# Performance work log

Hardware: AMD Instinct MI355X
Metric: run time of the kernel (lower is better)

## Reference

```python
import jax, jax.numpy as jnp
import numpy as np

RANK = 64          # rank
ENT_COMPS = 5      # ent_comps (1 time + 4 space components per rank slot)
REL_COMPS = 4      # rel_comps (quaternion / boost velocity)
N_ENT = 80000
N_REL = 500
B = 2000
INIT_SIZE = 0.001
SCALE = 1.0 / np.sqrt(RANK)
EPS = 1e-9


def _quat_mul(q, p):
    # Hamilton product of quaternions q, p: [..., 4] each, layout (w, x, y, z)
    qw, qx, qy, qz = q[..., 0], q[..., 1], q[..., 2], q[..., 3]
    pw, px, py, pz = p[..., 0], p[..., 1], p[..., 2], p[..., 3]
    return jnp.stack([
        qw * pw - qx * px - qy * py - qz * pz,
        qw * px + qx * pw + qy * pz - qz * py,
        qw * py - qx * pz + qy * pw + qz * px,
        qw * pz + qx * py - qy * px + qz * pw,
    ], axis=-1)


def lorentz_rotate(x, r):
    # x: [B, R, 5] Lorentz vectors (t, s4); r: [B, R, 4] rotation quaternion.
    # Spatial 4D isoclinic rotation via unit-quaternion left multiplication; time fixed.
    q = r * jax.lax.rsqrt(jnp.sum(r * r, axis=-1, keepdims=True) + EPS)
    t, s = x[..., :1], x[..., 1:]
    return jnp.concatenate([t, _quat_mul(q, s)], axis=-1)


def lorentz_boost(x, v):
    # x: [B, R, 5]; v: [B, R, 4] boost velocity (|v| < 1).
    t, s = x[..., :1], x[..., 1:]
    vn2 = jnp.clip(jnp.sum(v * v, axis=-1, keepdims=True), 0.0, 0.999)  # [B,R,1]
    gamma = jax.lax.rsqrt(1.0 - vn2)
    vs = jnp.sum(v * s, axis=-1, keepdims=True)
    t2 = gamma * (t + vs)
    s2 = s + (gamma * t + (gamma - 1.0) * vs / (vn2 + EPS)) * v
    return jnp.concatenate([t2, s2], axis=-1)


def setup_inputs() -> dict:
    key = jax.random.key(0)
    k = jax.random.split(key, 6)
    queries = jax.random.randint(k[0], (B, 3), 0, N_REL, dtype=jnp.int32)
    stru_entities = jax.random.normal(k[1], (N_ENT, 2 * RANK, ENT_COMPS), jnp.float32) * INIT_SIZE
    stru_rel_rotate = jax.random.normal(k[2], (N_REL, RANK, REL_COMPS), jnp.float32) * INIT_SIZE
    stru_rel_boosts = jax.random.normal(k[3], (N_REL, RANK, REL_COMPS), jnp.float32) * INIT_SIZE
    stru_atten = jax.random.normal(k[4], (N_REL, 1, ENT_COMPS * RANK), jnp.float32) * INIT_SIZE
    stru_rel_aux = jax.random.normal(k[5], (N_REL, 2, ENT_COMPS * RANK), jnp.float32) * INIT_SIZE
    return {
        "queries": queries,
        "stru_entities": stru_entities,
        "stru_rel_rotate": stru_rel_rotate,
        "stru_rel_boosts": stru_rel_boosts,
        "stru_atten": stru_atten,
        "stru_rel_aux": stru_rel_aux,
    }


def reference(queries, stru_entities, stru_rel_rotate, stru_rel_boosts, stru_atten, stru_rel_aux):
    b = queries.shape[0]
    D = ENT_COMPS * RANK  # 320
    h, r, t = queries[:, 0], queries[:, 1], queries[:, 2]

    slhs = stru_entities[h]                       # [B, 2R, 5]
    srhs = stru_entities[t]                       # [B, 2R, 5]
    lhs_re = slhs[:, :RANK]                       # [B, R, 5]
    lhs_im = slhs[:, RANK:].reshape(b, D)         # [B, D]
    rhs_re = srhs[:, :RANK].reshape(b, D)
    rhs_im = srhs[:, RANK:].reshape(b, D)

    rrot = stru_rel_rotate[r]                     # [B, R, 4]
    rboost = stru_rel_boosts[r]                   # [B, R, 4]
    atten = stru_atten[r]                         # [B, 1, D]
    aux = stru_rel_aux[r]                         # [B, 2, D]
    aux0, aux1 = aux[:, 0], aux[:, 1]

    to_re = stru_entities[:, :RANK].reshape(N_ENT, D)
    to_im = stru_entities[:, RANK:].reshape(N_ENT, D)

    rot = lorentz_rotate(lhs_re, rrot).reshape(b, D, 1)
    boo = lorentz_boost(lhs_re, rboost).reshape(b, D, 1)
    cands = jnp.concatenate([rot, boo], axis=-1)              # [B, D, 2]
    weights = jax.nn.softmax(jnp.matmul(atten * SCALE, cands), axis=-1)  # [B, 1, 2]
    lhs = jnp.sum(cands * weights, axis=-1)                   # [B, D]

    scores = (lhs * aux0 - lhs_im * aux1) @ to_re.T \
           + (lhs * aux1 + lhs_im * aux0) @ to_im.T           # [B, N_ENT]

    reg0 = jnp.sqrt(lhs_re.reshape(b, D) ** 2 + lhs_im ** 2)
    reg1 = jnp.sqrt(aux0 ** 2 + aux1 ** 2)
    reg2 = jnp.sqrt(rhs_re ** 2 + rhs_im ** 2) * (1.0 / 3.0)
    reg3 = jnp.sqrt(jnp.sum(rrot ** 2, axis=-1))
    reg4 = jnp.sqrt(jnp.sum(rboost ** 2, axis=-1))
    return scores, reg0, reg1, reg2, reg3, reg4
```

## Files before the change

kernel.cpp:

```cpp
#include <hip/hip_runtime.h>
#include <math.h>

#define RANK 64
#define D_DIM 320
#define K_DIM 640
#define N_ENT 80000
#define B_Q 2000
#define M_PAD 2048
#define NBLK_N 313
#define NT 10
#define SCALE_F 0.125f
#define EPS_F 1e-9f

#define OFF_SCORES 0ull
#define OFF_REG0 160000000ull
#define OFF_REG1 160640000ull
#define OFF_REG2 161280000ull
#define OFF_REG3 161920000ull
#define OFF_REG4 162048000ull

typedef __attribute__((ext_vector_type(8))) short short8v;
typedef __attribute__((ext_vector_type(4))) float floatx4;

typedef __attribute__((address_space(1))) const unsigned int gu32;
typedef __attribute__((address_space(3))) unsigned int lu32;

#define VMCNT4() asm volatile("s_waitcnt vmcnt(4)" ::: "memory")
#define VMCNT0() asm volatile("s_waitcnt vmcnt(0)" ::: "memory")
#define LGKM0()  asm volatile("s_waitcnt lgkmcnt(0)" ::: "memory")

static __device__ __forceinline__ unsigned short f2bf(float f) {
    union { float f; unsigned int u; } a; a.f = f;
    unsigned int u = a.u;
    u += 0x7FFFu + ((u >> 16) & 1u);
    return (unsigned short)(u >> 16);
}

static __device__ __forceinline__ void prep_row(
    int b, int lane,
    const int* __restrict__ q,
    const float* __restrict__ ent,
    const float* __restrict__ rrot_t,
    const float* __restrict__ rboost_t,
    const float* __restrict__ atten_t,
    const float* __restrict__ aux_t,
    unsigned short* __restrict__ X,
    float* __restrict__ out)
{
    unsigned short* Xrow = X + (size_t)b * K_DIM;

    if (b >= B_Q) {
        #pragma unroll
        for (int c = 0; c < 10; c++) Xrow[lane * 10 + c] = 0;
        return;
    }

    int h = q[3 * b + 0];
    int r = q[3 * b + 1];
    int t = q[3 * b + 2];

    const float* eh = ent + (size_t)h * K_DIM;
    const float* et = ent + (size_t)t * K_DIM;

    float4 rv = *(const float4*)(rrot_t + (size_t)r * 256 + lane * 4);
    float4 bv = *(const float4*)(rboost_t + (size_t)r * 256 + lane * 4);

    const float* xr = eh + lane * 5;
    float x0 = xr[0], x1 = xr[1], x2 = xr[2], x3 = xr[3], x4 = xr[4];

    float rr2 = rv.x * rv.x + rv.y * rv.y + rv.z * rv.z + rv.w * rv.w;
    float rb2 = bv.x * bv.x + bv.y * bv.y + bv.z * bv.z + bv.w * bv.w;

    float qinv = 1.0f / sqrtf(rr2 + EPS_F);
    float qw = rv.x * qinv, qx = rv.y * qinv, qy = rv.z * qinv, qz = rv.w * qinv;
    float pw = x1, px = x2, py = x3, pz = x4;
    float rot[5];
    rot[0] = x0;
    rot[1] = qw * pw - qx * px - qy * py - qz * pz;
    rot[2] = qw * px + qx * pw + qy * pz - qz * py;
    rot[3] = qw * py - qx * pz + qy * pw + qz * px;
    rot[4] = qw * pz + qx * py - qy * px + qz * pw;

    float vn2 = fminf(fmaxf(rb2, 0.0f), 0.999f);
    float sq = sqrtf(1.0f - vn2);
    float gamma = 1.0f / sq;
    float gm1 = vn2 / (sq * (1.0f + sq));
    float vs = bv.x * x1 + bv.y * x2 + bv.z * x3 + bv.w * x4;
    float boo[5];
    boo[0] = gamma * (x0 + vs);
    float coef = gamma * x0 + gm1 * vs / (vn2 + EPS_F);
    boo[1] = x1 + coef * bv.x;
    boo[2] = x2 + coef * bv.y;
    boo[3] = x3 + coef * bv.z;
    boo[4] = x4 + coef * bv.w;

    const float* at = atten_t + (size_t)r * D_DIM + lane * 5;
    float w0 = at[0] * rot[0] + at[1] * rot[1] + at[2] * rot[2] + at[3] * rot[3] + at[4] * rot[4];
    float w1 = at[0] * boo[0] + at[1] * boo[1] + at[2] * boo[2] + at[3] * boo[3] + at[4] * boo[4];
    #pragma unroll
    for (int off = 32; off; off >>= 1) {
        w0 += __shfl_xor(w0, off);
        w1 += __shfl_xor(w1, off);
    }
    w0 *= SCALE_F;
    w1 *= SCALE_F;
    float mx = fmaxf(w0, w1);
    float e0 = expf(w0 - mx), e1 = expf(w1 - mx);
    float inv = 1.0f / (e0 + e1);
    float wt0 = e0 * inv, wt1 = e1 * inv;

    const float* a0p = aux_t + (size_t)r * 640 + lane * 5;
    const float* a1p = a0p + D_DIM;
    float xre[5] = {x0, x1, x2, x3, x4};

    #pragma unroll
    for (int c = 0; c < 5; c++) {
        int d = lane * 5 + c;
        float lhs = wt0 * rot[c] + wt1 * boo[c];
        float im = eh[D_DIM + d];
        float a0 = a0p[c], a1 = a1p[c];
        Xrow[d]         = f2bf(lhs * a0 - im * a1);
        Xrow[D_DIM + d] = f2bf(lhs * a1 + im * a0);
        out[OFF_REG0 + (size_t)b * D_DIM + d] = sqrtf(xre[c] * xre[c] + im * im);
        out[OFF_REG1 + (size_t)b * D_DIM + d] = sqrtf(a0 * a0 + a1 * a1);
        float tre = et[d], tim = et[D_DIM + d];
        out[OFF_REG2 + (size_t)b * D_DIM + d] = sqrtf(tre * tre + tim * tim) * (1.0f / 3.0f);
    }
    out[OFF_REG3 + (size_t)b * RANK + lane] = sqrtf(rr2);
    out[OFF_REG4 + (size_t)b * RANK + lane] = sqrtf(rb2);
}

#define PREP_BLKS 512
#define CONV_BLKS 2048
__global__ __launch_bounds__(256) void prepconv_kernel(
    const int* __restrict__ q,
    const float* __restrict__ ent,
    const float* __restrict__ rrot_t,
    const float* __restrict__ rboost_t,
    const float* __restrict__ atten_t,
    const float* __restrict__ aux_t,
    unsigned short* __restrict__ X,
    unsigned short* __restrict__ Eb,
    float* __restrict__ out)
{
    if (blockIdx.x < PREP_BLKS) {
        int b = blockIdx.x * 4 + (threadIdx.x >> 6);
        prep_row(b, threadIdx.x & 63, q, ent, rrot_t, rboost_t, atten_t, aux_t, X, out);
    } else {
        const size_t n4 = (size_t)N_ENT * K_DIM / 4;
        size_t stride = (size_t)CONV_BLKS * 256;
        for (size_t v = (size_t)(blockIdx.x - PREP_BLKS) * 256 + threadIdx.x; v < n4; v += stride) {
            float4 f = ((const float4*)ent)[v];
            ushort4 u;
            u.x = f2bf(f.x); u.y = f2bf(f.y); u.z = f2bf(f.z); u.w = f2bf(f.w);
            ((ushort4*)Eb)[v] = u;
        }
    }
}

__global__ __launch_bounds__(64) void prep_kernel(
    const int* __restrict__ q, const float* __restrict__ ent,
    const float* __restrict__ rrot_t, const float* __restrict__ rboost_t,
    const float* __restrict__ atten_t, const float* __restrict__ aux_t,
    unsigned short* __restrict__ X, float* __restrict__ out)
{
    prep_row(blockIdx.x, threadIdx.x, q, ent, rrot_t, rboost_t, atten_t, aux_t, X, out);
}

__global__ __launch_bounds__(512, 1) void gemm256(
    const unsigned short* __restrict__ X,
    const unsigned short* __restrict__ Eb,
    float* __restrict__ C)
{
    __shared__ unsigned short lds[65536];

    const int tid = threadIdx.x;
    const int lane = tid & 63;
    const int wid = tid >> 6;
    const int wm = wid >> 2;
    const int wn = wid & 3;

    int bid = blockIdx.x;
    const int m0 = (bid & 7) * 256;
    const int n0 = (bid >> 3) * 256;

    const int fr = lane & 15;
    const int kq = lane >> 4;
    const int cbs8 = (kq ^ ((fr >> 1) & 3)) * 8;

    floatx4 acc[8][4];
    #pragma unroll
    for (int i = 0; i < 8; i++)
        #pragma unroll
        for (int j = 0; j < 4; j++) acc[i][j] = (floatx4)0.0f;

    const int srow = tid >> 2;
    const int scb = tid & 3;

    auto stage_ht = [&](int bufOff, int kt, int h) {
        const int mat = h & 1, kk = h >> 1;
        const int base = bufOff + mat * 16384 + kk * 8192;
        #pragma unroll
        for (int l = 0; l < 2; l++) {
            int row = srow + l * 128;
            int colg = kk * 32 + ((scb ^ ((row >> 1) & 3)) * 8);
            const unsigned short* gp;
            if (mat == 0) {
                gp = X + (size_t)(m0 + row) * K_DIM + kt * 64 + colg;
            } else {
                int grow = n0 + row;
                if (grow > N_ENT - 1) grow = N_ENT - 1;
                gp = Eb + (size_t)grow * K_DIM + kt * 64 + colg;
            }
            __builtin_amdgcn_global_load_lds((gu32*)gp,
                (lu32*)&lds[base + row * 32 + scb * 8], 16, 0, 0);
        }
    };

#define PHASE2(KK, WAITM, PF)                                                 \
    {                                                                         \
        const unsigned short* Ab_ = lds + bufo + (KK) * 8192;                 \
        const unsigned short* Bb_ = lds + bufo + 16384 + (KK) * 8192;         \
        short8v a_[8], b_[4];                                                 \
        _Pragma("unroll")                                                     \
        for (int i2 = 0; i2 < 8; i2++) {                                      \
            int row = wm * 128 + i2 * 16 + fr;                                \
            a_[i2] = *(const short8v*)&Ab_[row * 32 + cbs8];                  \
        }                                                                     \
        _Pragma("unroll")                                                     \
        for (int j = 0; j < 4; j++) {                                         \
            int row = wn * 64 + j * 16 + fr;                                  \
            b_[j] = *(const short8v*)&Bb_[row * 32 + cbs8];                   \
        }                                                                     \
        if (PF) {                                                             \
            stage_ht(nbo, t + 1, (KK) * 2 + 0);                               \
            stage_ht(nbo, t + 1, (KK) * 2 + 1);                               \
        }                                                                     \
        WAITM();                                                              \
        __builtin_amdgcn_s_barrier();                                         \
        LGKM0();                                                              \
        __builtin_amdgcn_sched_barrier(0);                                    \
        __builtin_amdgcn_s_setprio(1);                                        \
        _Pragma("unroll")                                                     \
        for (int i2 = 0; i2 < 8; i2++)                                        \
            _Pragma("unroll")                                                 \
            for (int j = 0; j < 4; j++)                                       \
                acc[i2][j] = __builtin_amdgcn_mfma_f32_16x16x32_bf16(         \
                    a_[i2], b_[j], acc[i2][j], 0, 0, 0);                      \
        __builtin_amdgcn_s_setprio(0);                                        \
        __builtin_amdgcn_s_barrier();                                         \
    }

    #pragma unroll
    for (int h = 0; h < 4; h++) stage_ht(0, 0, h);
    VMCNT0();
    __builtin_amdgcn_s_barrier();

    for (int t = 0; t < NT - 1; t++) {
        const int bufo = (t & 1) * 32768;
        const int nbo = bufo ^ 32768;
        PHASE2(0, VMCNT4, true)
        PHASE2(1, VMCNT4, true)
    }
    {
        const int t = NT - 1;
        const int bufo = (t & 1) * 32768;
        const int nbo = bufo ^ 32768;
        (void)nbo;
        PHASE2(0, VMCNT0, false)
        PHASE2(1, VMCNT0, false)
    }
#undef PHASE2

    const int rb = kq * 4;
    #pragma unroll
    for (int i = 0; i < 8; i++) {
        #pragma unroll
        for (int j = 0; j < 4; j++) {
            int row = m0 + wm * 128 + i * 16 + rb;
            int col = n0 + wn * 64 + j * 16 + fr;
            if (col < N_ENT) {
                #pragma unroll
                for (int r = 0; r < 4; r++) {
                    if (row + r < B_Q)
                        C[(size_t)(row + r) * N_ENT + col] = acc[i][j][r];
                }
            }
        }
    }
}

__global__ __launch_bounds__(256) void gemm_mfma_fb(
    const unsigned short* __restrict__ X,
    const float* __restrict__ Ef,
    float* __restrict__ C)
{
    __shared__ unsigned short As[128 * 32];
    __shared__ unsigned short Bs[128 * 32];

    const int tid = threadIdx.x;
    const int lane = tid & 63;
    const int wave = tid >> 6;
    const int wm = wave >> 1, wn = wave & 1;
    const int m0 = blockIdx.x * 128;
    const int n0 = blockIdx.y * 128;

    floatx4 acc[4][4];
    #pragma unroll
    for (int i = 0; i < 4; i++)
        #pragma unroll
        for (int j = 0; j < 4; j++) acc[i][j] = (floatx4)0.0f;

    const int srow = tid >> 2;
    const int scol = (tid & 3) * 8;
    const int fr = lane & 15;
    const int kb = (lane >> 4) * 8;
    const int brow_f = tid >> 1;
    const int bcol_f = (tid & 1) * 16;

    for (int k0 = 0; k0 < K_DIM; k0 += 32) {
        __syncthreads();
        #pragma unroll
        for (int r = 0; r < 2; r++) {
            const unsigned short* gp = X + (size_t)(m0 + srow + r * 64) * K_DIM + k0 + scol;
            __builtin_amdgcn_global_load_lds((gu32*)gp, (lu32*)(As + (size_t)(r * 64 + srow) * 32 + scol), 16, 0, 0);
        }
        {
            const float* ep = Ef + (size_t)(n0 + brow_f) * K_DIM + k0 + bcol_f;
            float4 f0 = *(const float4*)(ep);
            float4 f1 = *(const float4*)(ep + 4);
            float4 f2 = *(const float4*)(ep + 8);
            float4 f3 = *(const float4*)(ep + 12);
            short8v p0, p1;
            p0[0] = (short)f2bf(f0.x); p0[1] = (short)f2bf(f0.y);
            p0[2] = (short)f2bf(f0.z); p0[3] = (short)f2bf(f0.w);
            p0[4] = (short)f2bf(f1.x); p0[5] = (short)f2bf(f1.y);
            p0[6] = (short)f2bf(f1.z); p0[7] = (short)f2bf(f1.w);
            p1[0] = (short)f2bf(f2.x); p1[1] = (short)f2bf(f2.y);
            p1[2] = (short)f2bf(f2.z); p1[3] = (short)f2bf(f2.w);
            p1[4] = (short)f2bf(f3.x); p1[5] = (short)f2bf(f3.y);
            p1[6] = (short)f2bf(f3.z); p1[7] = (short)f2bf(f3.w);
            *(short8v*)(Bs + (size_t)brow_f * 32 + bcol_f) = p0;
            *(short8v*)(Bs + (size_t)brow_f * 32 + bcol_f + 8) = p1;
        }
        __syncthreads();

        short8v a[4], b[4];
        #pragma unroll
        for (int i = 0; i < 4; i++)
            a[i] = *(const short8v*)(As + (size_t)(wm * 64 + i * 16 + fr) * 32 + kb);
        #pragma unroll
        for (int j = 0; j < 4; j++)
            b[j] = *(const short8v*)(Bs + (size_t)(wn * 64 + j * 16 + fr) * 32 + kb);

        #pragma unroll
        for (int i = 0; i < 4; i++)
            #pragma unroll
            for (int j = 0; j < 4; j++)
                acc[i][j] = __builtin_amdgcn_mfma_f32_16x16x32_bf16(a[i], b[j], acc[i][j], 0, 0, 0);
    }

    const int rbase = (lane >> 4) * 4;
    #pragma unroll
    for (int i = 0; i < 4; i++) {
        #pragma unroll
        for (int j = 0; j < 4; j++) {
            int row = m0 + wm * 64 + i * 16 + rbase;
            int col = n0 + wn * 64 + j * 16 + fr;
            #pragma unroll
            for (int r = 0; r < 4; r++) {
                if (row + r < B_Q)
                    C[(size_t)(row + r) * N_ENT + col] = acc[i][j][r];
            }
        }
    }
}

extern "C" void kernel_launch(void* const* d_in, const int* in_sizes, int n_in,
                              void* d_out, int out_size, void* d_ws, size_t ws_size,
                              hipStream_t stream) {
    const int* queries = (const int*)d_in[0];
    const float* ent = (const float*)d_in[1];
    const float* rrot = (const float*)d_in[2];
    const float* rboost = (const float*)d_in[3];
    const float* atten = (const float*)d_in[4];
    const float* aux = (const float*)d_in[5];
    float* out = (float*)d_out;

    unsigned short* X = (unsigned short*)d_ws;
    const size_t offE = (size_t)M_PAD * K_DIM * 2;
    const size_t needE = (size_t)N_ENT * K_DIM * 2;
    unsigned short* Eb = (unsigned short*)((char*)d_ws + offE);
    bool pre = (ws_size >= offE + needE);

    if (pre) {
        prepconv_kernel<<<PREP_BLKS + CONV_BLKS, 256, 0, stream>>>(
            queries, ent, rrot, rboost, atten, aux, X, Eb, out);
        gemm256<<<8 * NBLK_N, 512, 0, stream>>>(X, Eb, out + OFF_SCORES);
    } else {
        prep_kernel<<<M_PAD, 64, 0, stream>>>(queries, ent, rrot, rboost, atten, aux, X, out);
        dim3 grid(M_PAD / 128, N_ENT / 128);
        gemm_mfma_fb<<<grid, 256, 0, stream>>>(X, ent, out + OFF_SCORES);
    }
}
```

Measured before the change: 411.0 us.

## Shrink GEMM tile to 256x128 with triple-buffered K=32 stages for higher occupancy

The bf16 MFMA GEMM changes from a 256x256 tile with a double-buffered K=64 pipeline to a 256x128 tile with a three-slot ring of K=32 stages, prefetching two stages ahead. LDS use drops from 128KB to 72KB and launch bounds ask for more resident blocks, so more waves can hide latency. N-boundary clamping is dropped because 80000 divides evenly by 128. In exchange, each block reuses less data (B-operand and X loaded twice as often per output) and synchronises more often per unit of K.

```diff
diff --git a/kernel.cpp b/kernel.cpp
--- a/kernel.cpp
+++ b/kernel.cpp
@@ -7,8 +7,7 @@
 #define N_ENT 80000
 #define B_Q 2000
 #define M_PAD 2048
-#define NBLK_N 313
-#define NT 10
+#define NT32 20
 #define SCALE_F 0.125f
 #define EPS_F 1e-9f
 
@@ -25,7 +24,7 @@
 typedef __attribute__((address_space(1))) const unsigned int gu32;
 typedef __attribute__((address_space(3))) unsigned int lu32;
 
-#define VMCNT4() asm volatile("s_waitcnt vmcnt(4)" ::: "memory")
+#define VMCNT3() asm volatile("s_waitcnt vmcnt(3)" ::: "memory")
 #define VMCNT0() asm volatile("s_waitcnt vmcnt(0)" ::: "memory")
 #define LGKM0()  asm volatile("s_waitcnt lgkmcnt(0)" ::: "memory")
 
@@ -167,124 +166,103 @@
     prep_row(blockIdx.x, threadIdx.x, q, ent, rrot_t, rboost_t, atten_t, aux_t, X, out);
 }
 
-__global__ __launch_bounds__(512, 1) void gemm256(
+__global__ __launch_bounds__(512, 4) void gemm256b(
     const unsigned short* __restrict__ X,
     const unsigned short* __restrict__ Eb,
     float* __restrict__ C)
 {
-    __shared__ unsigned short lds[65536];
+    __shared__ unsigned short lds[36864];
 
     const int tid = threadIdx.x;
     const int lane = tid & 63;
     const int wid = tid >> 6;
-    const int wm = wid >> 2;
-    const int wn = wid & 3;
-
-    int bid = blockIdx.x;
+    const int wm = wid >> 1;
+    const int wn = wid & 1;
+
+    const int bid = blockIdx.x;
     const int m0 = (bid & 7) * 256;
-    const int n0 = (bid >> 3) * 256;
+    const int n0 = (bid >> 3) * 128;
 
     const int fr = lane & 15;
     const int kq = lane >> 4;
     const int cbs8 = (kq ^ ((fr >> 1) & 3)) * 8;
 
-    floatx4 acc[8][4];
-    #pragma unroll
-    for (int i = 0; i < 8; i++)
+    floatx4 acc[4][4];
+    #pragma unroll
+    for (int i = 0; i < 4; i++)
         #pragma unroll
         for (int j = 0; j < 4; j++) acc[i][j] = (floatx4)0.0f;
 
+    int aoff[4], boff[4];
+    #pragma unroll
+    for (int i = 0; i < 4; i++) aoff[i] = (wm * 64 + i * 16 + fr) * 32 + cbs8;
+    #pragma unroll
+    for (int j = 0; j < 4; j++) boff[j] = 8192 + (wn * 64 + j * 16 + fr) * 32 + cbs8;
+
     const int srow = tid >> 2;
-    const int scb = tid & 3;
-
-    auto stage_ht = [&](int bufOff, int kt, int h) {
-        const int mat = h & 1, kk = h >> 1;
-        const int base = bufOff + mat * 16384 + kk * 8192;
-        #pragma unroll
-        for (int l = 0; l < 2; l++) {
-            int row = srow + l * 128;
-            int colg = kk * 32 + ((scb ^ ((row >> 1) & 3)) * 8);
-            const unsigned short* gp;
-            if (mat == 0) {
-                gp = X + (size_t)(m0 + row) * K_DIM + kt * 64 + colg;
-            } else {
-                int grow = n0 + row;
-                if (grow > N_ENT - 1) grow = N_ENT - 1;
-                gp = Eb + (size_t)grow * K_DIM + kt * 64 + colg;
-            }
-            __builtin_amdgcn_global_load_lds((gu32*)gp,
-                (lu32*)&lds[base + row * 32 + scb * 8], 16, 0, 0);
-        }
+    const int sslot = tid & 3;
+    const int scolg = (sslot ^ ((srow >> 1) & 3)) * 8;
+    const unsigned short* gA0 = X + (size_t)(m0 + srow) * K_DIM + scolg;
+    const unsigned short* gA1 = X + (size_t)(m0 + 128 + srow) * K_DIM + scolg;
+    const unsigned short* gB  = Eb + (size_t)(n0 + srow) * K_DIM + scolg;
+    const int ldst = tid * 8;
+
+    auto stage = [&](int bufS , int kt) {
+        const int base = bufS * 12288;
+        __builtin_amdgcn_global_load_lds((gu32*)(gA0 + kt * 32), (lu32*)&lds[base + ldst],        16, 0, 0);
+        __builtin_amdgcn_global_load_lds((gu32*)(gA1 + kt * 32), (lu32*)&lds[base + 4096 + ldst], 16, 0, 0);
+        __builtin_amdgcn_global_load_lds((gu32*)(gB  + kt * 32), (lu32*)&lds[base + 8192 + ldst], 16, 0, 0);
     };
 
-#define PHASE2(KK, WAITM, PF)                                                 \
+#define PHASE_BODY(BASE, STAGE_STMT, WAITM)                                   \
     {                                                                         \
-        const unsigned short* Ab_ = lds + bufo + (KK) * 8192;                 \
-        const unsigned short* Bb_ = lds + bufo + 16384 + (KK) * 8192;         \
-        short8v a_[8], b_[4];                                                 \
+        short8v a_[4], b_[4];                                                 \
         _Pragma("unroll")                                                     \
-        for (int i2 = 0; i2 < 8; i2++) {                                      \
-            int row = wm * 128 + i2 * 16 + fr;                                \
-            a_[i2] = *(const short8v*)&Ab_[row * 32 + cbs8];                  \
-        }                                                                     \
+        for (int i = 0; i < 4; i++) a_[i] = *(const short8v*)&lds[(BASE) + aoff[i]]; \
         _Pragma("unroll")                                                     \
-        for (int j = 0; j < 4; j++) {                                         \
-            int row = wn * 64 + j * 16 + fr;                                  \
-            b_[j] = *(const short8v*)&Bb_[row * 32 + cbs8];                   \
-        }                                                                     \
-        if (PF) {                                                             \
-            stage_ht(nbo, t + 1, (KK) * 2 + 0);                               \
-            stage_ht(nbo, t + 1, (KK) * 2 + 1);                               \
-        }                                                                     \
+        for (int j = 0; j < 4; j++) b_[j] = *(const short8v*)&lds[(BASE) + boff[j]]; \
+        STAGE_STMT;                                                           \
         WAITM();                                                              \
         __builtin_amdgcn_s_barrier();                                         \
         LGKM0();                                                              \
         __builtin_amdgcn_sched_barrier(0);                                    \
         __builtin_amdgcn_s_setprio(1);                                        \
         _Pragma("unroll")                                                     \
-        for (int i2 = 0; i2 < 8; i2++)                                        \
+        for (int i = 0; i < 4; i++)                                           \
             _Pragma("unroll")                                                 \
             for (int j = 0; j < 4; j++)                                       \
-                acc[i2][j] = __builtin_amdgcn_mfma_f32_16x16x32_bf16(         \
-                    a_[i2], b_[j], acc[i2][j], 0, 0, 0);                      \
+                acc[i][j] = __builtin_amdgcn_mfma_f32_16x16x32_bf16(          \
+                    a_[i], b_[j], acc[i][j], 0, 0, 0);                        \
         __builtin_amdgcn_s_setprio(0);                                        \
         __builtin_amdgcn_s_barrier();                                         \
     }
 
-    #pragma unroll
-    for (int h = 0; h < 4; h++) stage_ht(0, 0, h);
+    stage(0, 0);
+    stage(1, 1);
     VMCNT0();
     __builtin_amdgcn_s_barrier();
 
-    for (int t = 0; t < NT - 1; t++) {
-        const int bufo = (t & 1) * 32768;
-        const int nbo = bufo ^ 32768;
-        PHASE2(0, VMCNT4, true)
-        PHASE2(1, VMCNT4, true)
-    }
-    {
-        const int t = NT - 1;
-        const int bufo = (t & 1) * 32768;
-        const int nbo = bufo ^ 32768;
-        (void)nbo;
-        PHASE2(0, VMCNT0, false)
-        PHASE2(1, VMCNT0, false)
-    }
-#undef PHASE2
+    int bR = 0;
+    for (int t = 0; t < NT32 - 2; ++t) {
+        int bS = bR + 2; if (bS >= 3) bS -= 3;
+        PHASE_BODY(bR * 12288, stage(bS, t + 2), VMCNT3)
+        bR = (bR + 1 == 3) ? 0 : bR + 1;
+    }
+    PHASE_BODY(0, (void)0, VMCNT0)
+    PHASE_BODY(12288, (void)0, VMCNT0)
+#undef PHASE_BODY
 
     const int rb = kq * 4;
     #pragma unroll
-    for (int i = 0; i < 8; i++) {
+    for (int i = 0; i < 4; i++) {
         #pragma unroll
         for (int j = 0; j < 4; j++) {
-            int row = m0 + wm * 128 + i * 16 + rb;
+            int row = m0 + wm * 64 + i * 16 + rb;
             int col = n0 + wn * 64 + j * 16 + fr;
-            if (col < N_ENT) {
-                #pragma unroll
-                for (int r = 0; r < 4; r++) {
-                    if (row + r < B_Q)
-                        C[(size_t)(row + r) * N_ENT + col] = acc[i][j][r];
-                }
+            #pragma unroll
+            for (int r = 0; r < 4; r++) {
+                if (row + r < B_Q)
+                    C[(size_t)(row + r) * N_ENT + col] = acc[i][j][r];
             }
         }
     }
@@ -396,7 +374,7 @@
     if (pre) {
         prepconv_kernel<<<PREP_BLKS + CONV_BLKS, 256, 0, stream>>>(
             queries, ent, rrot, rboost, atten, aux, X, Eb, out);
-        gemm256<<<8 * NBLK_N, 512, 0, stream>>>(X, Eb, out + OFF_SCORES);
+        gemm256b<<<8 * 625, 512, 0, stream>>>(X, Eb, out + OFF_SCORES);
     } else {
         prep_kernel<<<M_PAD, 64, 0, stream>>>(queries, ent, rrot, rboost, atten, aux, X, out);
         dim3 grid(M_PAD / 128, N_ENT / 128);
```

Result: slower. 448.4 us (+9.1%).
